# Performance work log

Hardware: AMD Instinct MI355X
Metric: run time of the kernel (lower is better)

Reference implementation:

```python
import jax, jax.numpy as jnp
import numpy as np

# DSVT single-stage config (mmdet3d DSVT-Pillar, Waymo)
SPARSE_SHAPE = (468, 468, 1)            # (x, y, z)
WIN_SHAPES = [(12, 12, 1), (24, 24, 1)]  # base window, hybrid window (hybrid_factor=[2,2,1])
SHIFTS = [(0, 0, 0), (6, 6, 0)]          # shift_list per shift id
SET_SIZE = 36
NUM_BLOCKS = 4
DIM = 192
BN_EPS = 1e-5


def get_window_coors(coors, sparse_shape, window_shape, shift):
    ssx, ssy, ssz = sparse_shape
    wx, wy, wz = window_shape
    mx = int(np.ceil(ssx / wx) + 1)
    my = int(np.ceil(ssy / wy) + 1)
    mz = int(np.ceil(ssz / wz) + 1)
    sx, sy, sz = shift
    if ssz == wz:
        sz = 0
    scx = coors[:, 3] + sx
    scy = coors[:, 2] + sy
    scz = coors[:, 1] + sz
    batch_win_inds = (coors[:, 0] * (mx * my * mz)
                      + (scx // wx) * my * mz + (scy // wy) * mz + (scz // wz))
    coors_in_win = jnp.stack([scz % wz, scy % wy, scx % wx], axis=-1)  # (z, y, x)
    return batch_win_inds, coors_in_win


def get_inner_win_inds(win_inds):
    # rank of each voxel inside its window (stable order), like get_inner_win_inds
    n = win_inds.shape[0]
    order = jnp.argsort(win_inds)  # jnp.argsort is stable
    sw = win_inds[order]
    ar = jnp.arange(n, dtype=win_inds.dtype)
    is_start = jnp.concatenate([jnp.ones((1,), bool), sw[1:] != sw[:-1]])
    start = jax.lax.cummax(jnp.where(is_start, ar, 0), axis=0)
    return jnp.zeros(n, win_inds.dtype).at[order].set(ar - start)


def get_set_single_shift(batch_win_inds, coors_in_win, window_shape, set_size):
    wx, wy, wz = window_shape
    max_voxel = wx * wy * wz
    n = batch_win_inds.shape[0]
    uniq, contig = jnp.unique(batch_win_inds, return_inverse=True)
    contig = contig.reshape(-1).astype(jnp.int32)
    win_num = int(uniq.shape[0])
    vnum_per_win = jnp.bincount(contig, length=win_num).astype(jnp.int32)
    setnum_per_win = (vnum_per_win + set_size - 1) // set_size  # ceil
    # get_continous_inds
    set_win_inds = jnp.repeat(jnp.arange(win_num, dtype=jnp.int32), setnum_per_win)
    excl = jnp.concatenate([jnp.zeros((1,), jnp.int32),
                            jnp.cumsum(setnum_per_win)[:-1].astype(jnp.int32)])
    set_inds_in_win = jnp.arange(set_win_inds.shape[0], dtype=jnp.int32) - excl[set_win_inds]

    # Eq.3 of DSVT: evenly spread the voxels of each window over its sets
    base_idx = jnp.arange(set_size, dtype=jnp.int32)
    num = (set_inds_in_win[:, None] * set_size + base_idx) * vnum_per_win[set_win_inds][:, None]
    den = (setnum_per_win[set_win_inds] * set_size)[:, None]
    select_idx = num // den + set_win_inds[:, None] * max_voxel  # [set_num, set_size]

    inner = get_inner_win_inds(contig)
    order1 = jnp.argsort(contig * max_voxel + inner)

    z = coors_in_win[:, 0].astype(jnp.int32)
    y = coors_in_win[:, 1].astype(jnp.int32)
    x = coors_in_win[:, 2].astype(jnp.int32)

    def partition(key):
        order2 = jnp.argsort(key)
        inner_s = jnp.full((n,), -1, jnp.int32).at[order2].set(inner[order1])
        in_batch = inner_s + max_voxel * contig
        padding = jnp.full((win_num * max_voxel,), -1, jnp.int32).at[in_batch].set(
            jnp.arange(n, dtype=jnp.int32))
        return padding[select_idx]

    key_sorty = contig * max_voxel + y * (wx * wz) + x * wz + z
    key_sortx = contig * max_voxel + x * (wy * wz) + y * wz + z
    return jnp.stack([partition(key_sorty), partition(key_sortx)], axis=0)


def set_mask(set_voxel_inds):
    prefix = jnp.roll(set_voxel_inds, 1, axis=-1).at[:, :, 0].set(-1)
    return set_voxel_inds == prefix


def compute_locations(voxel_coords):
    infos, locs = [], []
    win_x, win_y = WIN_SHAPES[0][0], WIN_SHAPES[0][1]  # pos-embed uses base window, 2D (win_z==1)
    for s in range(2):
        bwi, ciw = get_window_coors(voxel_coords, SPARSE_SHAPE, WIN_SHAPES[s], SHIFTS[s])
        infos.append((bwi, ciw))
        xx = ciw[:, 2].astype(jnp.float32) - win_x / 2
        yy = ciw[:, 1].astype(jnp.float32) - win_y / 2
        locs.append(jnp.stack([xx, yy], axis=-1))
    return infos, jnp.stack(locs)  # [2, N, 2]


def _pos_embed(w1, b1, g, bt, w2, b2, loc):
    # Linear -> BatchNorm1d (train-mode batch stats) -> ReLU -> Linear
    h = loc @ w1 + b1
    mu = h.mean(0)
    var = h.var(0)
    h = (h - mu) * jax.lax.rsqrt(var + BN_EPS) * g + bt
    return jnp.maximum(h, 0.0) @ w2 + b2


def setup_inputs() -> dict:
    key = jax.random.key(0)
    B, NPB, GX, GY = 2, 30000, 468, 468
    rng = np.random.default_rng(0)
    coords = []
    for b in range(B):
        lin = rng.choice(GX * GY, size=NPB, replace=False)  # unique occupied pillars
        coords.append(np.stack([np.full(NPB, b), np.zeros(NPB), lin // GX, lin % GX], axis=1))
    voxel_coords = jnp.asarray(np.concatenate(coords, 0), dtype=jnp.int32)  # (bid, z, y, x)
    N = B * NPB
    K = 2 * NUM_BLOCKS
    ks = jax.random.split(key, 3)
    return {
        'voxel_features': jax.random.normal(ks[0], (N, DIM), jnp.float32),
        'voxel_coords': voxel_coords,
        'pe_w1': jax.random.normal(ks[1], (K, 2, DIM), jnp.float32) * 0.02,
        'pe_b1': jnp.zeros((K, DIM), jnp.float32),
        'pe_gamma': jnp.ones((K, DIM), jnp.float32),
        'pe_beta': jnp.zeros((K, DIM), jnp.float32),
        'pe_w2': jax.random.normal(ks[2], (K, DIM, DIM), jnp.float32) * 0.02,
        'pe_b2': jnp.zeros((K, DIM), jnp.float32),
    }


def reference(voxel_features, voxel_coords, pe_w1, pe_b1, pe_gamma, pe_beta, pe_w2, pe_b2):
    infos, locs = compute_locations(voxel_coords)
    set_inds0 = get_set_single_shift(infos[0][0], infos[0][1], WIN_SHAPES[0], SET_SIZE)
    set_inds1 = get_set_single_shift(infos[1][0], infos[1][1], WIN_SHAPES[1], SET_SIZE)
    mask0 = set_mask(set_inds0)
    mask1 = set_mask(set_inds1)
    # 4 blocks x 2 shifts learned position embeddings; location depends only on shift
    loc_k = locs[jnp.arange(2 * NUM_BLOCKS) % 2]  # [8, N, 2]
    pos_embeds = jax.vmap(_pos_embed)(pe_w1, pe_b1, pe_gamma, pe_beta, pe_w2, pe_b2, loc_k)
    return (voxel_features, voxel_coords, set_inds0, mask0, set_inds1, mask1, pos_embeds)
```

## Files before the change

kernel.cpp:

```cpp
#include <hip/hip_runtime.h>
#include <stdint.h>

#define DIM 192
#define SET_SIZE 36

#define W0 6400
#define MV0 144
#define W1 1764
#define MV1 576

#define CAP_S0 6144
#define CAP_S1 4096

#define OFF_CNT0     0
#define OFF_CNT1     6400
#define OFF_MOM      8164
#define OFF_S0       8174
#define OFF_S1       8175
#define OFF_ZERO_END 8176
#define OFF_SETBASE0 8192
#define OFF_SETBASE1 14592
#define OFF_SETWIN0  16356
#define OFF_SETWIN1  22500
#define OFF_CELL0    26596
#define OFF_CELL1    86596
#define OFF_SLOTY0   146596
#define OFF_SLOTX0   1068196
#define OFF_SLOTY1   1989796
#define OFF_SLOTX1   3005860
#define OFF_TABLE    4021924
#define WS_TOTAL     4906660

__global__ void voxel_pass(const int* __restrict__ coords, int N, int* __restrict__ ws) {
    int v = blockIdx.x * blockDim.x + threadIdx.x;
    __shared__ int sm[10];
    if (threadIdx.x < 10) sm[threadIdx.x] = 0;
    __syncthreads();
    if (v < N) {
        int b = coords[v * 4 + 0];
        int z = coords[v * 4 + 1];
        int y = coords[v * 4 + 2];
        int x = coords[v * 4 + 3];
        int xin0 = x % 12, yin0 = y % 12;
        int w0 = b * 3200 + (x / 12) * 80 + (y / 12) * 2 + z;
        atomicAdd(&ws[OFF_CNT0 + w0], 1);
        ws[OFF_SLOTY0 + w0 * MV0 + yin0 * 12 + xin0] = v;
        ws[OFF_SLOTX0 + w0 * MV0 + xin0 * 12 + yin0] = v;
        ws[OFF_CELL0 + v] = yin0 * 12 + xin0;
        int sx = x + 6, sy = y + 6;
        int xin1 = sx % 24, yin1 = sy % 24;
        int w1 = b * 882 + (sx / 24) * 42 + (sy / 24) * 2 + z;
        atomicAdd(&ws[OFF_CNT1 + w1], 1);
        ws[OFF_SLOTY1 + w1 * MV1 + yin1 * 24 + xin1] = v;
        ws[OFF_SLOTX1 + w1 * MV1 + xin1 * 24 + yin1] = v;
        ws[OFF_CELL1 + v] = yin1 * 24 + xin1;
        int xx0 = xin0 - 6, yy0 = yin0 - 6;
        int xx1 = xin1 - 6, yy1 = yin1 - 6;
        atomicAdd(&sm[0], xx0); atomicAdd(&sm[1], yy0);
        atomicAdd(&sm[2], xx0 * xx0); atomicAdd(&sm[3], yy0 * yy0); atomicAdd(&sm[4], xx0 * yy0);
        atomicAdd(&sm[5], xx1); atomicAdd(&sm[6], yy1);
        atomicAdd(&sm[7], xx1 * xx1); atomicAdd(&sm[8], yy1 * yy1); atomicAdd(&sm[9], xx1 * yy1);
    }
    __syncthreads();
    if (threadIdx.x < 10) atomicAdd(&ws[OFF_MOM + threadIdx.x], sm[threadIdx.x]);
}

__global__ void scan_sets(const int* __restrict__ cnt, int W,
                          int* __restrict__ setBase, int* __restrict__ setWin,
                          int* __restrict__ S_out, int cap) {
    __shared__ int sm[256];
    int tid = threadIdx.x;
    int chunk = (W + 255) >> 8;
    int lo = tid * chunk;
    int hi = lo + chunk; if (hi > W) hi = W; if (lo > W) lo = W;
    int local = 0;
    for (int w = lo; w < hi; w++) local += (cnt[w] + SET_SIZE - 1) / SET_SIZE;
    sm[tid] = local;
    __syncthreads();
    for (int off = 1; off < 256; off <<= 1) {
        int t = (tid >= off) ? sm[tid - off] : 0;
        __syncthreads();
        sm[tid] += t;
        __syncthreads();
    }
    int base = sm[tid] - local;
    if (tid == 255) {
        int S = sm[255];
        if (S > cap) S = cap;
        *S_out = S;
    }
    for (int w = lo; w < hi; w++) {
        setBase[w] = base;
        int sn = (cnt[w] + SET_SIZE - 1) / SET_SIZE;
        for (int s = 0; s < sn; s++) {
            int idx = base + s;
            if (idx < cap) setWin[idx] = w;
        }
        base += sn;
    }
}

__global__ void compact_windows(int* __restrict__ slotY, int* __restrict__ slotX, int MV) {
    int w = blockIdx.x;
    int lane = threadIdx.x;
    for (int pass = 0; pass < 2; pass++) {
        int* slot = pass ? slotX : slotY;
        int base = 0;
        for (int p0 = 0; p0 < MV; p0 += 64) {
            int p = p0 + lane;
            int v = (p < MV) ? slot[(size_t)w * MV + p] : -1;
            bool occ = v >= 0;
            unsigned long long m = __ballot(occ);
            int rank = __popcll(m & ((1ull << lane) - 1ull));
            if (occ) slot[(size_t)w * MV + base + rank] = v;
            base += __popcll(m);
        }
    }
}

__global__ void write_sets(const int* __restrict__ S_ptr, const int* __restrict__ setWin,
                           const int* __restrict__ setBase, const int* __restrict__ cnt,
                           const int* __restrict__ sortedY, const int* __restrict__ sortedX,
                           int MV, int cap, float* __restrict__ outArea,
                           const int* __restrict__ S_prev ) {
    long long tid = (long long)blockIdx.x * blockDim.x + threadIdx.x;
    int S = *S_ptr;
    int j = (int)(tid % SET_SIZE);
    long long t = tid / SET_SIZE;
    int q = (int)(t % cap);
    int branch = (int)(t / cap);
    if (branch >= 2 || q >= S) return;
    long long sOff = 0;
    if (S_prev) sOff = 4LL * SET_SIZE * (long long)(*S_prev);
    int w = setWin[q];
    int i = q - setBase[w];
    int vnum = cnt[w];
    int setnum = (vnum + SET_SIZE - 1) / SET_SIZE;
    int den = setnum * SET_SIZE;
    int r  = ((i * SET_SIZE + j) * vnum) / den;
    int rp = (j > 0) ? (((i * SET_SIZE + j - 1) * vnum) / den) : -1;
    const int* sorted = branch ? sortedX : sortedY;
    int vox = sorted[(size_t)w * MV + r];
    long long idx = (long long)branch * S * SET_SIZE + (long long)q * SET_SIZE + j;
    outArea[sOff + idx] = (float)vox;
    outArea[sOff + 2LL * S * SET_SIZE + idx] = (r == rp) ? 1.0f : 0.0f;
}

__global__ void build_table(const float* __restrict__ w1, const float* __restrict__ gamma,
                            const float* __restrict__ beta, const float* __restrict__ w2,
                            const float* __restrict__ b2, const int* __restrict__ mom,
                            float* __restrict__ table, int N) {
    int k = blockIdx.x / MV1;
    int cell = blockIdx.x % MV1;
    int shift = k & 1;
    int wdim = shift ? 24 : 12;
    if (cell >= wdim * wdim) return;
    int j = threadIdx.x;
    const int* m = mom + shift * 5;
    double invN = 1.0 / (double)N;
    double mx = m[0] * invN, my = m[1] * invN;
    double vx = m[2] * invN - mx * mx;
    double vy = m[3] * invN - my * my;
    double cxy = m[4] * invN - mx * my;
    int cy = cell / wdim, cx = cell % wdim;
    double xx = (double)(cx - 6), yy = (double)(cy - 6);
    float w10 = w1[(k * 2 + 0) * DIM + j];
    float w11 = w1[(k * 2 + 1) * DIM + j];
    double var = (double)w10 * w10 * vx + (double)w11 * w11 * vy + 2.0 * (double)w10 * w11 * cxy;
    double rs = 1.0 / sqrt(var + 1e-5);
    double hn = ((xx - mx) * (double)w10 + (yy - my) * (double)w11) * rs * (double)gamma[k * DIM + j]
                + (double)beta[k * DIM + j];
    float hr = hn > 0.0 ? (float)hn : 0.0f;
    __shared__ float sh[DIM];
    sh[j] = hr;
    __syncthreads();
    float acc = b2[k * DIM + j];
    const float* w2k = w2 + (size_t)k * DIM * DIM;
    #pragma unroll 8
    for (int i = 0; i < DIM; i++) acc += sh[i] * w2k[i * DIM + j];
    table[((size_t)k * MV1 + cell) * DIM + j] = acc;
}

__global__ void scatter_pe(const float4* __restrict__ table, const int* __restrict__ cell0,
                           const int* __restrict__ cell1, float4* __restrict__ out, int N) {
    long long tid = (long long)blockIdx.x * blockDim.x + threadIdx.x;
    long long total = 8LL * N * (DIM / 4);
    if (tid >= total) return;
    int q = (int)(tid % (DIM / 4));
    long long t = tid / (DIM / 4);
    int v = (int)(t % N);
    int k = (int)(t / N);
    int cell = (k & 1) ? cell1[v] : cell0[v];
    out[tid] = table[((size_t)k * MV1 + cell) * (DIM / 4) + q];
}

__global__ void coords_to_float(const int* __restrict__ c, float* __restrict__ o, int n) {
    int i = blockIdx.x * blockDim.x + threadIdx.x;
    if (i < n) o[i] = (float)c[i];
}

extern "C" void kernel_launch(void* const* d_in, const int* in_sizes, int n_in,
                              void* d_out, int out_size, void* d_ws, size_t ws_size,
                              hipStream_t stream) {
    const float* feat  = (const float*)d_in[0];
    const int* coords  = (const int*)d_in[1];
    const float* w1    = (const float*)d_in[2];
    const float* gamma = (const float*)d_in[4];
    const float* beta  = (const float*)d_in[5];
    const float* w2    = (const float*)d_in[6];
    const float* b2    = (const float*)d_in[7];
    int N = in_sizes[1] / 4;
    int* ws = (int*)d_ws;
    float* out = (float*)d_out;

    hipMemsetAsync(ws, 0, (size_t)OFF_ZERO_END * sizeof(int), stream);
    hipMemsetAsync(ws + OFF_SLOTY0, 0xFF, (size_t)(OFF_TABLE - OFF_SLOTY0) * sizeof(int), stream);

    voxel_pass<<<(N + 255) / 256, 256, 0, stream>>>(coords, N, ws);

    scan_sets<<<1, 256, 0, stream>>>(ws + OFF_CNT0, W0, ws + OFF_SETBASE0, ws + OFF_SETWIN0,
                                     ws + OFF_S0, CAP_S0);
    scan_sets<<<1, 256, 0, stream>>>(ws + OFF_CNT1, W1, ws + OFF_SETBASE1, ws + OFF_SETWIN1,
                                     ws + OFF_S1, CAP_S1);

    compact_windows<<<W0, 64, 0, stream>>>(ws + OFF_SLOTY0, ws + OFF_SLOTX0, MV0);
    compact_windows<<<W1, 64, 0, stream>>>(ws + OFF_SLOTY1, ws + OFF_SLOTX1, MV1);

    long long off2 = (long long)N * DIM + (long long)N * 4;
    {
        long long threads = 2LL * CAP_S0 * SET_SIZE;
        write_sets<<<(int)((threads + 255) / 256), 256, 0, stream>>>(
            ws + OFF_S0, ws + OFF_SETWIN0, ws + OFF_SETBASE0, ws + OFF_CNT0,
            ws + OFF_SLOTY0, ws + OFF_SLOTX0, MV0, CAP_S0, out + off2, nullptr);
    }
    {
        long long threads = 2LL * CAP_S1 * SET_SIZE;
        write_sets<<<(int)((threads + 255) / 256), 256, 0, stream>>>(
            ws + OFF_S1, ws + OFF_SETWIN1, ws + OFF_SETBASE1, ws + OFF_CNT1,
            ws + OFF_SLOTY1, ws + OFF_SLOTX1, MV1, CAP_S1, out + off2, ws + OFF_S0);
    }

    build_table<<<8 * MV1, DIM, 0, stream>>>(w1, gamma, beta, w2, b2,
                                             ws + OFF_MOM, (float*)(ws + OFF_TABLE), N);

    long long off6 = (long long)out_size - 8LL * N * DIM;
    {
        long long t4 = 8LL * N * (DIM / 4);
        scatter_pe<<<(int)((t4 + 255) / 256), 256, 0, stream>>>(
            (const float4*)(ws + OFF_TABLE), ws + OFF_CELL0, ws + OFF_CELL1,
            (float4*)(out + off6), N);
    }

    coords_to_float<<<(N * 4 + 255) / 256, 256, 0, stream>>>(coords, out + (long long)N * DIM, N * 4);
    hipMemcpyAsync(out, feat, (size_t)N * DIM * sizeof(float), hipMemcpyDeviceToDevice, stream);
}
```

Before: 539.7 us.

## Merge per-shift kernels, drop z dimension from window layout, fuse coords conversion

Result: faster. 520.5 us (-3.6%).

```diff
diff --git a/kernel.cpp b/kernel.cpp
--- a/kernel.cpp
+++ b/kernel.cpp
@@ -4,52 +4,58 @@
 #define DIM 192
 #define SET_SIZE 36
 
-#define W0 6400
+#define W0 3200
 #define MV0 144
-#define W1 1764
+#define W1 882
 #define MV1 576
 
 #define CAP_S0 6144
 #define CAP_S1 4096
 
 #define OFF_CNT0     0
-#define OFF_CNT1     6400
-#define OFF_MOM      8164
-#define OFF_S0       8174
-#define OFF_S1       8175
-#define OFF_ZERO_END 8176
-#define OFF_SETBASE0 8192
-#define OFF_SETBASE1 14592
-#define OFF_SETWIN0  16356
-#define OFF_SETWIN1  22500
-#define OFF_CELL0    26596
-#define OFF_CELL1    86596
-#define OFF_SLOTY0   146596
-#define OFF_SLOTX0   1068196
-#define OFF_SLOTY1   1989796
-#define OFF_SLOTX1   3005860
-#define OFF_TABLE    4021924
-#define WS_TOTAL     4906660
-
-__global__ void voxel_pass(const int* __restrict__ coords, int N, int* __restrict__ ws) {
+#define OFF_CNT1     3200
+#define OFF_MOM      4082
+#define OFF_S0       4092
+#define OFF_S1       4093
+#define OFF_ZERO_END 4096
+#define OFF_SETBASE0 4096
+#define OFF_SETBASE1 7296
+#define OFF_SETWIN0  8192
+#define OFF_SETWIN1  14336
+#define OFF_CELL0    18432
+#define OFF_CELL1    78432
+#define OFF_SLOTY0   138432
+#define OFF_SLOTX0   599232
+#define OFF_SLOTY1   1060032
+#define OFF_SLOTX1   1568064
+#define OFF_TABLE    2076096
+#define WS_TOTAL     2960832
+
+#define SLOT4 ((OFF_TABLE - OFF_SLOTY0) / 4)
+
+__global__ void init_ws(int* __restrict__ ws) {
+    int t = blockIdx.x * 256 + threadIdx.x;
+    if (t < OFF_ZERO_END / 4) ((int4*)ws)[t] = make_int4(0, 0, 0, 0);
+    if (t < SLOT4) ((int4*)(ws + OFF_SLOTY0))[t] = make_int4(-1, -1, -1, -1);
+}
+
+__global__ void voxel_pass(const int4* __restrict__ coords, int N, int* __restrict__ ws) {
     int v = blockIdx.x * blockDim.x + threadIdx.x;
     __shared__ int sm[10];
     if (threadIdx.x < 10) sm[threadIdx.x] = 0;
     __syncthreads();
     if (v < N) {
-        int b = coords[v * 4 + 0];
-        int z = coords[v * 4 + 1];
-        int y = coords[v * 4 + 2];
-        int x = coords[v * 4 + 3];
+        int4 c = coords[v];
+        int b = c.x, y = c.z, x = c.w;
         int xin0 = x % 12, yin0 = y % 12;
-        int w0 = b * 3200 + (x / 12) * 80 + (y / 12) * 2 + z;
+        int w0 = b * 1600 + (x / 12) * 40 + (y / 12);
         atomicAdd(&ws[OFF_CNT0 + w0], 1);
         ws[OFF_SLOTY0 + w0 * MV0 + yin0 * 12 + xin0] = v;
         ws[OFF_SLOTX0 + w0 * MV0 + xin0 * 12 + yin0] = v;
         ws[OFF_CELL0 + v] = yin0 * 12 + xin0;
         int sx = x + 6, sy = y + 6;
         int xin1 = sx % 24, yin1 = sy % 24;
-        int w1 = b * 882 + (sx / 24) * 42 + (sy / 24) * 2 + z;
+        int w1 = b * 441 + (sx / 24) * 21 + (sy / 24);
         atomicAdd(&ws[OFF_CNT1 + w1], 1);
         ws[OFF_SLOTY1 + w1 * MV1 + yin1 * 24 + xin1] = v;
         ws[OFF_SLOTX1 + w1 * MV1 + xin1 * 24 + yin1] = v;
@@ -65,10 +71,15 @@
     if (threadIdx.x < 10) atomicAdd(&ws[OFF_MOM + threadIdx.x], sm[threadIdx.x]);
 }
 
-__global__ void scan_sets(const int* __restrict__ cnt, int W,
-                          int* __restrict__ setBase, int* __restrict__ setWin,
-                          int* __restrict__ S_out, int cap) {
+__global__ void scan_both(int* __restrict__ ws) {
     __shared__ int sm[256];
+    int shift = blockIdx.x;
+    const int W = shift ? W1 : W0;
+    const int cap = shift ? CAP_S1 : CAP_S0;
+    const int* cnt = ws + (shift ? OFF_CNT1 : OFF_CNT0);
+    int* setBase = ws + (shift ? OFF_SETBASE1 : OFF_SETBASE0);
+    int* setWin  = ws + (shift ? OFF_SETWIN1 : OFF_SETWIN0);
+    int* S_out   = ws + (shift ? OFF_S1 : OFF_S0);
     int tid = threadIdx.x;
     int chunk = (W + 255) >> 8;
     int lo = tid * chunk;
@@ -100,8 +111,13 @@
     }
 }
 
-__global__ void compact_windows(int* __restrict__ slotY, int* __restrict__ slotX, int MV) {
-    int w = blockIdx.x;
+__global__ void compact_all(int* __restrict__ ws) {
+    int bw = blockIdx.x;
+    int shift = (bw >= W0) ? 1 : 0;
+    int w = shift ? (bw - W0) : bw;
+    int MV = shift ? MV1 : MV0;
+    int* slotY = ws + (shift ? OFF_SLOTY1 : OFF_SLOTY0);
+    int* slotX = ws + (shift ? OFF_SLOTX1 : OFF_SLOTX0);
     int lane = threadIdx.x;
     for (int pass = 0; pass < 2; pass++) {
         int* slot = pass ? slotX : slotY;
@@ -118,20 +134,27 @@
     }
 }
 
-__global__ void write_sets(const int* __restrict__ S_ptr, const int* __restrict__ setWin,
-                           const int* __restrict__ setBase, const int* __restrict__ cnt,
-                           const int* __restrict__ sortedY, const int* __restrict__ sortedX,
-                           int MV, int cap, float* __restrict__ outArea,
-                           const int* __restrict__ S_prev ) {
+__global__ void write_sets_both(const int* __restrict__ ws, float* __restrict__ outArea) {
     long long tid = (long long)blockIdx.x * blockDim.x + threadIdx.x;
-    int S = *S_ptr;
-    int j = (int)(tid % SET_SIZE);
-    long long t = tid / SET_SIZE;
-    int q = (int)(t % cap);
-    int branch = (int)(t / cap);
+    const long long T0 = 2LL * CAP_S0 * SET_SIZE;
+    const long long T1 = 2LL * CAP_S1 * SET_SIZE;
+    int shift = tid >= T0;
+    long long t = shift ? tid - T0 : tid;
+    if (shift && t >= T1) return;
+    int cap = shift ? CAP_S1 : CAP_S0;
+    int MV = shift ? MV1 : MV0;
+    const int* setWin  = ws + (shift ? OFF_SETWIN1 : OFF_SETWIN0);
+    const int* setBase = ws + (shift ? OFF_SETBASE1 : OFF_SETBASE0);
+    const int* cnt     = ws + (shift ? OFF_CNT1 : OFF_CNT0);
+    const int* slotY   = ws + (shift ? OFF_SLOTY1 : OFF_SLOTY0);
+    const int* slotX   = ws + (shift ? OFF_SLOTX1 : OFF_SLOTX0);
+    int S = ws[shift ? OFF_S1 : OFF_S0];
+    int j = (int)(t % SET_SIZE);
+    long long u = t / SET_SIZE;
+    int q = (int)(u % cap);
+    int branch = (int)(u / cap);
     if (branch >= 2 || q >= S) return;
-    long long sOff = 0;
-    if (S_prev) sOff = 4LL * SET_SIZE * (long long)(*S_prev);
+    long long sOff = shift ? 4LL * SET_SIZE * (long long)ws[OFF_S0] : 0;
     int w = setWin[q];
     int i = q - setBase[w];
     int vnum = cnt[w];
@@ -139,7 +162,7 @@
     int den = setnum * SET_SIZE;
     int r  = ((i * SET_SIZE + j) * vnum) / den;
     int rp = (j > 0) ? (((i * SET_SIZE + j - 1) * vnum) / den) : -1;
-    const int* sorted = branch ? sortedX : sortedY;
+    const int* sorted = branch ? slotX : slotY;
     int vox = sorted[(size_t)w * MV + r];
     long long idx = (long long)branch * S * SET_SIZE + (long long)q * SET_SIZE + j;
     outArea[sOff + idx] = (float)vox;
@@ -182,8 +205,14 @@
 }
 
 __global__ void scatter_pe(const float4* __restrict__ table, const int* __restrict__ cell0,
-                           const int* __restrict__ cell1, float4* __restrict__ out, int N) {
+                           const int* __restrict__ cell1, float4* __restrict__ outPe,
+                           const int4* __restrict__ coords, float4* __restrict__ outCoords,
+                           int N) {
     long long tid = (long long)blockIdx.x * blockDim.x + threadIdx.x;
+    if (tid < N) {
+        int4 c = coords[tid];
+        outCoords[tid] = make_float4((float)c.x, (float)c.y, (float)c.z, (float)c.w);
+    }
     long long total = 8LL * N * (DIM / 4);
     if (tid >= total) return;
     int q = (int)(tid % (DIM / 4));
@@ -191,12 +220,7 @@
     int v = (int)(t % N);
     int k = (int)(t / N);
     int cell = (k & 1) ? cell1[v] : cell0[v];
-    out[tid] = table[((size_t)k * MV1 + cell) * (DIM / 4) + q];
-}
-
-__global__ void coords_to_float(const int* __restrict__ c, float* __restrict__ o, int n) {
-    int i = blockIdx.x * blockDim.x + threadIdx.x;
-    if (i < n) o[i] = (float)c[i];
+    outPe[tid] = table[((size_t)k * MV1 + cell) * (DIM / 4) + q];
 }
 
 extern "C" void kernel_launch(void* const* d_in, const int* in_sizes, int n_in,
@@ -213,31 +237,18 @@
     int* ws = (int*)d_ws;
     float* out = (float*)d_out;
 
-    hipMemsetAsync(ws, 0, (size_t)OFF_ZERO_END * sizeof(int), stream);
-    hipMemsetAsync(ws + OFF_SLOTY0, 0xFF, (size_t)(OFF_TABLE - OFF_SLOTY0) * sizeof(int), stream);
-
-    voxel_pass<<<(N + 255) / 256, 256, 0, stream>>>(coords, N, ws);
-
-    scan_sets<<<1, 256, 0, stream>>>(ws + OFF_CNT0, W0, ws + OFF_SETBASE0, ws + OFF_SETWIN0,
-                                     ws + OFF_S0, CAP_S0);
-    scan_sets<<<1, 256, 0, stream>>>(ws + OFF_CNT1, W1, ws + OFF_SETBASE1, ws + OFF_SETWIN1,
-                                     ws + OFF_S1, CAP_S1);
-
-    compact_windows<<<W0, 64, 0, stream>>>(ws + OFF_SLOTY0, ws + OFF_SLOTX0, MV0);
-    compact_windows<<<W1, 64, 0, stream>>>(ws + OFF_SLOTY1, ws + OFF_SLOTX1, MV1);
+    init_ws<<<(SLOT4 + 255) / 256, 256, 0, stream>>>(ws);
+
+    voxel_pass<<<(N + 255) / 256, 256, 0, stream>>>((const int4*)coords, N, ws);
+
+    scan_both<<<2, 256, 0, stream>>>(ws);
+
+    compact_all<<<W0 + W1, 64, 0, stream>>>(ws);
 
     long long off2 = (long long)N * DIM + (long long)N * 4;
     {
-        long long threads = 2LL * CAP_S0 * SET_SIZE;
-        write_sets<<<(int)((threads + 255) / 256), 256, 0, stream>>>(
-            ws + OFF_S0, ws + OFF_SETWIN0, ws + OFF_SETBASE0, ws + OFF_CNT0,
-            ws + OFF_SLOTY0, ws + OFF_SLOTX0, MV0, CAP_S0, out + off2, nullptr);
-    }
-    {
-        long long threads = 2LL * CAP_S1 * SET_SIZE;
-        write_sets<<<(int)((threads + 255) / 256), 256, 0, stream>>>(
-            ws + OFF_S1, ws + OFF_SETWIN1, ws + OFF_SETBASE1, ws + OFF_CNT1,
-            ws + OFF_SLOTY1, ws + OFF_SLOTX1, MV1, CAP_S1, out + off2, ws + OFF_S0);
+        long long threads = 2LL * (CAP_S0 + CAP_S1) * SET_SIZE;
+        write_sets_both<<<(int)((threads + 255) / 256), 256, 0, stream>>>(ws, out + off2);
     }
 
     build_table<<<8 * MV1, DIM, 0, stream>>>(w1, gamma, beta, w2, b2,
@@ -248,9 +259,9 @@
         long long t4 = 8LL * N * (DIM / 4);
         scatter_pe<<<(int)((t4 + 255) / 256), 256, 0, stream>>>(
             (const float4*)(ws + OFF_TABLE), ws + OFF_CELL0, ws + OFF_CELL1,
-            (float4*)(out + off6), N);
-    }
-
-    coords_to_float<<<(N * 4 + 255) / 256, 256, 0, stream>>>(coords, out + (long long)N * DIM, N * 4);
+            (float4*)(out + off6), (const int4*)coords,
+            (float4*)(out + (long long)N * DIM), N);
+    }
+
     hipMemcpyAsync(out, feat, (size_t)N * DIM * sizeof(float), hipMemcpyDeviceToDevice, stream);
 }
```
